# Kernel tuning notes

Hardware: AMD Instinct MI355X
Metric: run time of the kernel (lower is better)

The kernel has to match this reference:

```python
import jax, jax.numpy as jnp
import numpy as np

D_MODEL = 1024
N_HEADS = 16
HEAD_DIM = D_MODEL // N_HEADS


def setup_inputs() -> dict:
    key = jax.random.key(0)
    k_x, k_qkv, k_out = jax.random.split(key, 3)
    B, T = 4, 2048
    x = jax.random.normal(k_x, (B, T, D_MODEL), dtype=jnp.float32)
    # nn.Linear weight is (out, in); we store transposed (in, out) for x @ W
    s = 1.0 / np.sqrt(D_MODEL)
    W_qkv = jax.random.uniform(k_qkv, (D_MODEL, 3 * D_MODEL), dtype=jnp.float32, minval=-s, maxval=s)
    W_out = jax.random.uniform(k_out, (D_MODEL, D_MODEL), dtype=jnp.float32, minval=-s, maxval=s)
    return {"x": x, "W_qkv": W_qkv, "W_out": W_out}


def reference(x, W_qkv, W_out):
    B, T, C = x.shape
    H, Dh = N_HEADS, HEAD_DIM
    qkv = x @ W_qkv                                   # (B,T,3C)
    q, k, v = jnp.split(qkv, 3, axis=-1)
    # (B,T,C) -> (B,H,T,Dh)
    def split_heads(t):
        return t.reshape(B, T, H, Dh).transpose(0, 2, 1, 3)
    q, k, v = split_heads(q), split_heads(k), split_heads(v)
    scale = 1.0 / np.sqrt(Dh).astype(np.float32)
    scores = jnp.einsum('bhqd,bhkd->bhqk', q, k) * scale  # (B,H,T,T)
    causal = jnp.triu(jnp.ones((T, T), dtype=bool), k=1)   # True above diag
    scores = jnp.where(causal, -jnp.inf, scores)
    attn = jax.nn.softmax(scores, axis=-1)
    out = jnp.einsum('bhqk,bhkd->bhqd', attn, v)       # (B,H,T,Dh)
    out = out.transpose(0, 2, 1, 3).reshape(B, T, C)
    return out @ W_out
```

## Files before the change

### kernel.cpp

```cpp
#include <hip/hip_runtime.h>
#include <stdint.h>

#define T_ 2048
#define BB_ 4

typedef __bf16 bf16x8 __attribute__((ext_vector_type(8)));
typedef float f32x4 __attribute__((ext_vector_type(4)));
typedef unsigned short u16x8 __attribute__((ext_vector_type(8)));
typedef unsigned int u32x2 __attribute__((ext_vector_type(2)));
typedef unsigned int u32x4 __attribute__((ext_vector_type(4)));

__device__ __forceinline__ unsigned short f2b(float f) {
    unsigned int u = __builtin_bit_cast(unsigned int, f);
    return (unsigned short)((u + 0x7fffu + ((u >> 16) & 1u)) >> 16);
}

__device__ __forceinline__ unsigned cvt_pk(float lo, float hi) {
    unsigned r;
    asm("v_cvt_pk_bf16_f32 %0, %1, %2" : "=v"(r) : "v"(lo), "v"(hi));
    return r;
}

__device__ __forceinline__ void gload16(const void* g, const void* lds) {
    __builtin_amdgcn_global_load_lds(
        (__attribute__((address_space(1))) void*)(uintptr_t)g,
        (__attribute__((address_space(3))) void*)(uintptr_t)(unsigned int)(uintptr_t)lds,
        16, 0, 0);
}

__device__ __forceinline__ bf16x8 ld_b8(const unsigned short* p) {
    return *(const bf16x8*)p;
}

#define MFMA16(a, b, c) __builtin_amdgcn_mfma_f32_16x16x32_bf16((a), (b), (c), 0, 0, 0)
#define SB() __builtin_amdgcn_sched_barrier(0)

__device__ __forceinline__ void cvtT_body(const float* __restrict__ W,
                                          unsigned short* __restrict__ WT, int K,
                                          int N, int bid, int tid,
                                          unsigned short (*t_)[72]) {
    const int nt = bid % (N / 64), kt = bid / (N / 64);
    const int r = tid >> 2, c = (tid & 3) * 16;
    const float* src = W + (size_t)(kt * 64 + r) * N + nt * 64 + c;
#pragma unroll
    for (int j = 0; j < 16; j += 4) {
        float4 v = *(const float4*)(src + j);
        t_[r][c + j + 0] = f2b(v.x);
        t_[r][c + j + 1] = f2b(v.y);
        t_[r][c + j + 2] = f2b(v.z);
        t_[r][c + j + 3] = f2b(v.w);
    }
    __syncthreads();
    unsigned short* dst = WT + (size_t)(nt * 64 + r) * K + kt * 64 + c;
#pragma unroll
    for (int j = 0; j < 16; ++j) dst[j] = t_[c + j][r];
}

__global__ __launch_bounds__(256) void k_prep(
    const float* __restrict__ x, const float* __restrict__ Wqkv,
    const float* __restrict__ Wout, unsigned short* __restrict__ xb,
    unsigned short* __restrict__ wqkvT, unsigned short* __restrict__ woutT) {
    __shared__ unsigned short t_[64][72];
    const int bid = blockIdx.x, tid = threadIdx.x;
    if (bid < 768) {
        cvtT_body(Wqkv, wqkvT, 1024, 3072, bid, tid, t_);
    } else if (bid < 1024) {
        cvtT_body(Wout, woutT, 1024, 1024, bid - 768, tid, t_);
    } else {
        int i = ((bid - 1024) * 256 + tid) * 4;
        const int stride = 2048 * 256 * 4;
        for (; i < BB_ * T_ * 1024; i += stride) {
            const float4 v = *(const float4*)(x + i);
            *(ushort4*)(xb + i) = make_ushort4(f2b(v.x), f2b(v.y), f2b(v.z), f2b(v.w));
        }
    }
}

__global__ __launch_bounds__(512, 4) void k_gemm32(
    const unsigned short* __restrict__ A, const unsigned short* __restrict__ Bt,
    unsigned short* __restrict__ qkv, unsigned short* __restrict__ vt2) {
    constexpr int K = 1024, NT = K / 32;
    __shared__ unsigned short Abuf[3][8192];
    __shared__ unsigned short Bbuf[3][4096];
    const int tid = threadIdx.x;
    const int lane = tid & 63, wid = tid >> 6;
    const int wr = wid >> 1, wc = wid & 1;
    const int l4 = lane >> 4, l15 = lane & 15;
    const int m0 = blockIdx.y * 256, n0 = blockIdx.x * 128;

    int arow[2], acol[2];
#pragma unroll
    for (int c = 0; c < 2; ++c) {
        const int lb = c * 8192 + tid * 16;
        const int r2 = lb >> 7;
        const int w = (lb & 127) ^ ((r2 & 7) << 4);
        arow[c] = r2 * 2 + (w >> 6);
        acol[c] = (w & 63) >> 1;
    }
    int brow, bcol;
    {
        const int lb = tid * 16;
        const int r2 = lb >> 7;
        const int w = (lb & 127) ^ ((r2 & 7) << 4);
        brow = r2 * 2 + (w >> 6);
        bcol = (w & 63) >> 1;
    }

    f32x4 acc[4][4] = {};

    auto STAGE = [&](int t, int d) {
        gload16(A + (size_t)(m0 + arow[0]) * K + t * 32 + acol[0], &Abuf[d][tid * 8]);
        gload16(A + (size_t)(m0 + arow[1]) * K + t * 32 + acol[1],
                &Abuf[d][4096 + tid * 8]);
        gload16(Bt + (size_t)(n0 + brow) * K + t * 32 + bcol, &Bbuf[d][tid * 8]);
    };

    auto rd = [&](const unsigned short* base, int R) {
        int byte = (R >> 1) * 128 + (R & 1) * 64 + l4 * 16;
        byte ^= ((R >> 1) & 7) << 4;
        return (const unsigned short*)((const char*)base + byte);
    };

    STAGE(0, 0);
    STAGE(1, 1);
    int d = 0;
    for (int t = 0; t < NT; ++t) {
        if (t == NT - 1)
            asm volatile("s_waitcnt vmcnt(0)" ::: "memory");
        else
            asm volatile("s_waitcnt vmcnt(3)" ::: "memory");
        SB();
        __builtin_amdgcn_s_barrier();
        SB();
        const int dn = (d + 2 >= 3) ? d - 1 : d + 2;
        if (t + 2 < NT) STAGE(t + 2, dn);
        SB();
        bf16x8 af[4], bfr[4];
#pragma unroll
        for (int m = 0; m < 4; ++m)
            af[m] = ld_b8(rd(&Abuf[d][0], wr * 64 + m * 16 + l15));
#pragma unroll
        for (int n = 0; n < 4; ++n)
            bfr[n] = ld_b8(rd(&Bbuf[d][0], wc * 64 + n * 16 + l15));
        __builtin_amdgcn_s_setprio(1);
#pragma unroll
        for (int m = 0; m < 4; ++m)
#pragma unroll
            for (int n = 0; n < 4; ++n)
                acc[m][n] = MFMA16(af[m], bfr[n], acc[m][n]);
        __builtin_amdgcn_s_setprio(0);
        d = (d + 1 == 3) ? 0 : d + 1;
    }

    const int crow0 = m0 + wr * 64 + l4 * 4;
    const int ccol0 = n0 + wc * 64 + l15;
    if (n0 >= 2048) {
#pragma unroll
        for (int m = 0; m < 4; ++m)
#pragma unroll
            for (int n = 0; n < 4; ++n) {
                const int row = crow0 + m * 16;
                const int c = ccol0 + n * 16 - 2048;
                const int b = row >> 11, tt = row & 2047;
                const int h = c >> 6, dh = c & 63;
                ushort4 o;
                o.x = f2b(acc[m][n][0]);
                o.y = f2b(acc[m][n][1]);
                o.z = f2b(acc[m][n][2]);
                o.w = f2b(acc[m][n][3]);
                *(ushort4*)(vt2 + (size_t)(b * 16 + h) * 131072 + (tt >> 2) * 256 +
                            dh * 4) = o;
            }
    } else {
#pragma unroll
        for (int m = 0; m < 4; ++m)
#pragma unroll
            for (int n = 0; n < 4; ++n)
#pragma unroll
                for (int r = 0; r < 4; ++r)
                    qkv[(size_t)(crow0 + m * 16 + r) * 3072 + ccol0 + n * 16] =
                        f2b(acc[m][n][r]);
    }
}

__global__ __launch_bounds__(512, 2) void k_gemm256(
    const unsigned short* __restrict__ A, const unsigned short* __restrict__ Bt,
    float* __restrict__ Cv) {
    constexpr int K = 1024, NT = K / 64, NCOLS = 1024;
    __shared__ unsigned short Abuf[3][2][8192];
    __shared__ unsigned short Bbuf[3][8192];
    const int tid = threadIdx.x;
    const int lane = tid & 63, wid = tid >> 6;
    const int wr = wid >> 1, wc = wid & 1;
    const int l4 = lane >> 4, l15 = lane & 15;
    const int m0 = blockIdx.y * 256, n0 = blockIdx.x * 128;

    const int se0 = tid * 8, se1 = tid * 8 + 4096;
    const int r0_ = se0 >> 6, c0_ = (se0 & 63) ^ ((r0_ & 7) << 3);
    const int r1_ = se1 >> 6, c1_ = (se1 & 63) ^ ((r1_ & 7) << 3);

    f32x4 acc[4][4] = {};

    auto STAGE1 = [&](int t, int d) {
        const unsigned short* as = A + (size_t)m0 * K + t * 64;
        gload16(as + (size_t)r0_ * K + c0_, &Abuf[d][0][se0]);
        gload16(as + (size_t)r1_ * K + c1_, &Abuf[d][0][se1]);
        const unsigned short* bs = Bt + (size_t)n0 * K + t * 64;
        gload16(bs + (size_t)r0_ * K + c0_, &Bbuf[d][se0]);
    };
    auto STAGE2 = [&](int t, int d) {
        const unsigned short* as = A + (size_t)(m0 + 128) * K + t * 64;
        gload16(as + (size_t)r0_ * K + c0_, &Abuf[d][1][se0]);
        gload16(as + (size_t)r1_ * K + c1_, &Abuf[d][1][se1]);
        const unsigned short* bs = Bt + (size_t)n0 * K + t * 64;
        gload16(bs + (size_t)r1_ * K + c1_, &Bbuf[d][se1]);
    };

    auto swz = [](const unsigned short* base, int row, int col) {
        int byte = row * 128 + col * 2;
        byte ^= (row & 7) << 4;
        return (const unsigned short*)((const char*)base + byte);
    };

    STAGE1(0, 0);
    STAGE2(0, 0);
    STAGE1(1, 1);
    STAGE2(1, 1);
    int d = 0;
    for (int t = 0; t < NT; ++t) {
        if (t == NT - 1)
            asm volatile("s_waitcnt vmcnt(0)" ::: "memory");
        else
            asm volatile("s_waitcnt vmcnt(6)" ::: "memory");
        SB();
        __builtin_amdgcn_s_barrier();
        SB();
        const int dn = (d + 2 >= 3) ? d - 1 : d + 2;
        if (t + 2 < NT) STAGE1(t + 2, dn);
        SB();
        const unsigned short* Ah = &Abuf[d][wr >> 1][0];
        const unsigned short* Bh = &Bbuf[d][0];
        bf16x8 af[2][4], bfr[2][4];
#pragma unroll
        for (int ks = 0; ks < 2; ++ks) {
#pragma unroll
            for (int m = 0; m < 4; ++m)
                af[ks][m] =
                    ld_b8(swz(Ah, (wr & 1) * 64 + m * 16 + l15, ks * 32 + l4 * 8));
#pragma unroll
            for (int n = 0; n < 4; ++n)
                bfr[ks][n] = ld_b8(swz(Bh, wc * 64 + n * 16 + l15, ks * 32 + l4 * 8));
        }
        __builtin_amdgcn_s_setprio(1);
#pragma unroll
        for (int m = 0; m < 4; ++m)
#pragma unroll
            for (int n = 0; n < 4; ++n)
                acc[m][n] = MFMA16(af[0][m], bfr[0][n], acc[m][n]);
        __builtin_amdgcn_s_setprio(0);
        SB();
        if (t + 2 < NT) STAGE2(t + 2, dn);
        SB();
        __builtin_amdgcn_s_setprio(1);
#pragma unroll
        for (int m = 0; m < 4; ++m)
#pragma unroll
            for (int n = 0; n < 4; ++n)
                acc[m][n] = MFMA16(af[1][m], bfr[1][n], acc[m][n]);
        __builtin_amdgcn_s_setprio(0);
        d = (d + 1 == 3) ? 0 : d + 1;
    }

    const int crow0 = m0 + wr * 64 + l4 * 4;
    const int ccol0 = n0 + wc * 64 + l15;
#pragma unroll
    for (int m = 0; m < 4; ++m)
#pragma unroll
        for (int n = 0; n < 4; ++n)
#pragma unroll
            for (int r = 0; r < 4; ++r)
                Cv[(size_t)(crow0 + m * 16 + r) * NCOLS + ccol0 + n * 16] =
                    acc[m][n][r];
}

__global__ __launch_bounds__(512) void k_attn(const unsigned short* __restrict__ qkv,
                                              const unsigned short* __restrict__ vt2,
                                              unsigned short* __restrict__ ao) {
    __shared__ unsigned short Ks[2 * 4096];
    __shared__ unsigned short Vs[2 * 4096];
    const int bh = blockIdx.x & 63;
    const int p = blockIdx.x >> 6;
    const int b = bh >> 4, h = bh & 15;
    const int tid = threadIdx.x, lane = tid & 63, w = tid >> 6;
    const int l4 = lane >> 4, l15 = lane & 15;
    const int wrow = w * 16 + l15;

    const int sr0 = w * 8 + (lane >> 3);
    const int scol = 8 * ((lane & 7) ^ (lane >> 3));
    const unsigned short* Kg = qkv + (size_t)(b * T_) * 3072 + 1024 + h * 64;

    const unsigned short* Vg = vt2 + (size_t)bh * 131072;
    const int sv = w * 2 + (lane >> 5);
    const unsigned short* vsrcw =
        Vg + (4 * (sv & 3) + (sv >> 2)) * 256 + (lane & 31) * 8;

    const u32x4 onesw = {0x3f803f80u, 0x3f803f80u, 0x3f803f80u, 0x3f803f80u};
    const bf16x8 ones = __builtin_bit_cast(bf16x8, onesw);

    for (int half = 0; half < 2; ++half) {
        const int qq = half ? p : 15 - p;

        const unsigned short* qb =
            qkv + (size_t)(b * T_ + qq * 128 + wrow) * 3072 + h * 64;
        bf16x8 qf0, qf1;
        {
            const bf16x8 r0 = ld_b8(qb + l4 * 8);
            const bf16x8 r1 = ld_b8(qb + 32 + l4 * 8);
#pragma unroll
            for (int j = 0; j < 8; ++j) {
                qf0[j] = (__bf16)((float)r0[j] * 0.18033688f);
                qf1[j] = (__bf16)((float)r1[j] * 0.18033688f);
            }
        }

        f32x4 o[4] = {};
        f32x4 o_l = {};

        auto STAGE = [&](int kt, int bi) {
            gload16(Kg + (size_t)(kt * 64 + sr0) * 3072 + scol,
                    Ks + bi * 4096 + w * 512);
            gload16(vsrcw + (size_t)kt * 4096, Vs + bi * 4096 + w * 512);
        };

        auto COMPUTE = [&](int bi, int dk) {
            const unsigned short* Kb = Ks + bi * 4096;
            const unsigned short* Vb = Vs + bi * 4096;
            float tv[4][4];
            __builtin_amdgcn_s_setprio(1);
#pragma unroll
            for (int i = 0; i < 4; ++i) {
                const int key = i * 16 + l15;
                const int sw = (key & 7) << 4;
                const bf16x8 kf0 = ld_b8(Kb + (key * 128 + ((l4 * 16) ^ sw)) / 2);
                const bf16x8 kf1 = ld_b8(Kb + (key * 128 + ((l4 * 16 + 64) ^ sw)) / 2);
                f32x4 sacc = {};
                sacc = MFMA16(kf0, qf0, sacc);
                sacc = MFMA16(kf1, qf1, sacc);
#pragma unroll
                for (int r = 0; r < 4; ++r) tv[i][r] = sacc[r];
            }
            __builtin_amdgcn_s_setprio(0);
            if (dk >= 0) {
                const int base = dk * 64 - wrow;
#pragma unroll
                for (int i = 0; i < 4; ++i)
#pragma unroll
                    for (int r = 0; r < 4; ++r)
                        if (base + i * 16 + l4 * 4 + r > 0) tv[i][r] = -1e30f;
            }
            unsigned pw[8];
#pragma unroll
            for (int i = 0; i < 4; ++i) {
                float pv[4];
#pragma unroll
                for (int r = 0; r < 4; ++r) pv[r] = __builtin_amdgcn_exp2f(tv[i][r]);
                pw[i * 2 + 0] = cvt_pk(pv[0], pv[1]);
                pw[i * 2 + 1] = cvt_pk(pv[2], pv[3]);
            }
            __builtin_amdgcn_s_setprio(1);
#pragma unroll
            for (int st = 0; st < 2; ++st) {
                const u32x4 pk = {pw[st * 4 + 0], pw[st * 4 + 1], pw[st * 4 + 2],
                                  pw[st * 4 + 3]};
                const bf16x8 pf = __builtin_bit_cast(bf16x8, pk);
                o_l = MFMA16(pf, ones, o_l);
#pragma unroll
                for (int ni = 0; ni < 4; ++ni) {
                    const unsigned short* vb =
                        Vb + (l4 * 4 + st * 2) * 256 + (ni * 16 + l15) * 4;
                    const u32x2 va = *(const u32x2*)vb;
                    const u32x2 vc = *(const u32x2*)(vb + 256);
                    const u32x4 vv = {va.x, va.y, vc.x, vc.y};
                    const bf16x8 vf = __builtin_bit_cast(bf16x8, vv);
                    o[ni] = MFMA16(pf, vf, o[ni]);
                }
            }
            __builtin_amdgcn_s_setprio(0);
        };

        const int NTI = 2 * qq + 1;
        __syncthreads();
        STAGE(0, 0);
        __syncthreads();
        for (int kt = 0; kt < NTI; ++kt) {
            STAGE(kt + 1, (kt + 1) & 1);
            COMPUTE(kt & 1, kt - 2 * qq);
            __syncthreads();
        }
        COMPUTE(NTI & 1, 1);

        unsigned short* aop =
            ao + (size_t)(b * T_ + qq * 128 + w * 16) * 1024 + h * 64;
#pragma unroll
        for (int r = 0; r < 4; ++r) {
            const float inv = 1.0f / o_l[r];
#pragma unroll
            for (int ni = 0; ni < 4; ++ni)
                aop[(size_t)(l4 * 4 + r) * 1024 + ni * 16 + l15] = f2b(o[ni][r] * inv);
        }
    }
}

extern "C" void kernel_launch(void* const* d_in, const int* in_sizes, int n_in,
                              void* d_out, int out_size, void* d_ws, size_t ws_size,
                              hipStream_t stream) {
    (void)in_sizes; (void)n_in; (void)out_size; (void)ws_size;
    const float* x = (const float*)d_in[0];
    const float* Wqkv = (const float*)d_in[1];
    const float* Wout = (const float*)d_in[2];
    char* ws = (char*)d_ws;
    unsigned short* xb = (unsigned short*)(ws + 0);
    unsigned short* wqkvT = (unsigned short*)(ws + 16777216);
    unsigned short* woutT = (unsigned short*)(ws + 23068672);
    unsigned short* qkvb = (unsigned short*)(ws + 25165824);
    unsigned short* vt2 = (unsigned short*)(ws + 75497472);
    unsigned short* ao = (unsigned short*)(ws + 92274688);

    k_prep<<<3072, 256, 0, stream>>>(x, Wqkv, Wout, xb, wqkvT, woutT);
    k_gemm32<<<dim3(24, 32), 512, 0, stream>>>(xb, wqkvT, qkvb, vt2);
    k_attn<<<512, 512, 0, stream>>>(qkvb, vt2, ao);
    k_gemm256<<<dim3(8, 32), 512, 0, stream>>>(ao, woutT, (float*)d_out);
}
```

Measured before the change: 143.9 us.

## Retile QKV GEMM to 128x192 blocks with a 2x4 wave layout

Changes the QKV projection GEMM tile from 256x128 to 128x192, giving 1024 blocks instead of 768, with 8 waves arranged 2x4, each computing 64x48. The staging loads become uneven: only the first four waves issue the extra B load, and the waitcnt depth is set per wave to match. The epilogue now decides per 16-column fragment whether to write the V-transposed layout, because a 192-wide tile can straddle the Q/K and V boundary. The goal is better wave-quantisation across CUs, at the cost of lower arithmetic intensity per tile and divergent load counts between waves.

```diff
diff --git a/kernel.cpp b/kernel.cpp
--- a/kernel.cpp
+++ b/kernel.cpp
@@ -76,43 +76,43 @@
     }
 }
 
-__global__ __launch_bounds__(512, 4) void k_gemm32(
+__global__ __launch_bounds__(512, 4) void k_gemm192(
     const unsigned short* __restrict__ A, const unsigned short* __restrict__ Bt,
     unsigned short* __restrict__ qkv, unsigned short* __restrict__ vt2) {
     constexpr int K = 1024, NT = K / 32;
-    __shared__ unsigned short Abuf[3][8192];
-    __shared__ unsigned short Bbuf[3][4096];
+    __shared__ unsigned short Abuf[3][4096];
+    __shared__ unsigned short Bbuf[3][6144];
     const int tid = threadIdx.x;
     const int lane = tid & 63, wid = tid >> 6;
-    const int wr = wid >> 1, wc = wid & 1;
+    const int wm = wid >> 2, wn = wid & 3;
     const int l4 = lane >> 4, l15 = lane & 15;
-    const int m0 = blockIdx.y * 256, n0 = blockIdx.x * 128;
-
-    int arow[2], acol[2];
-#pragma unroll
-    for (int c = 0; c < 2; ++c) {
-        const int lb = c * 8192 + tid * 16;
-        const int r2 = lb >> 7;
-        const int w = (lb & 127) ^ ((r2 & 7) << 4);
-        arow[c] = r2 * 2 + (w >> 6);
-        acol[c] = (w & 63) >> 1;
-    }
-    int brow, bcol;
+    const int m0 = blockIdx.y * 128, n0 = blockIdx.x * 192;
+
+    int ar, ac;
     {
         const int lb = tid * 16;
         const int r2 = lb >> 7;
         const int w = (lb & 127) ^ ((r2 & 7) << 4);
-        brow = r2 * 2 + (w >> 6);
-        bcol = (w & 63) >> 1;
-    }
-
-    f32x4 acc[4][4] = {};
+        ar = r2 * 2 + (w >> 6);
+        ac = (w & 63) >> 1;
+    }
+    int br1, bc1;
+    {
+        const int lb = 8192 + tid * 16;
+        const int r2 = lb >> 7;
+        const int w = (lb & 127) ^ ((r2 & 7) << 4);
+        br1 = r2 * 2 + (w >> 6);
+        bc1 = (w & 63) >> 1;
+    }
+
+    f32x4 acc[4][3] = {};
 
     auto STAGE = [&](int t, int d) {
-        gload16(A + (size_t)(m0 + arow[0]) * K + t * 32 + acol[0], &Abuf[d][tid * 8]);
-        gload16(A + (size_t)(m0 + arow[1]) * K + t * 32 + acol[1],
-                &Abuf[d][4096 + tid * 8]);
-        gload16(Bt + (size_t)(n0 + brow) * K + t * 32 + bcol, &Bbuf[d][tid * 8]);
+        gload16(A + (size_t)(m0 + ar) * K + t * 32 + ac, &Abuf[d][tid * 8]);
+        gload16(Bt + (size_t)(n0 + ar) * K + t * 32 + ac, &Bbuf[d][tid * 8]);
+        if (wid < 4)
+            gload16(Bt + (size_t)(n0 + br1) * K + t * 32 + bc1,
+                    &Bbuf[d][4096 + tid * 8]);
     };
 
     auto rd = [&](const unsigned short* base, int R) {
@@ -125,44 +125,48 @@
     STAGE(1, 1);
     int d = 0;
     for (int t = 0; t < NT; ++t) {
-        if (t == NT - 1)
+        if (t == NT - 1) {
             asm volatile("s_waitcnt vmcnt(0)" ::: "memory");
-        else
+        } else if (wid < 4) {
             asm volatile("s_waitcnt vmcnt(3)" ::: "memory");
+        } else {
+            asm volatile("s_waitcnt vmcnt(2)" ::: "memory");
+        }
         SB();
         __builtin_amdgcn_s_barrier();
         SB();
         const int dn = (d + 2 >= 3) ? d - 1 : d + 2;
         if (t + 2 < NT) STAGE(t + 2, dn);
         SB();
-        bf16x8 af[4], bfr[4];
+        bf16x8 af[4], bfr[3];
 #pragma unroll
         for (int m = 0; m < 4; ++m)
-            af[m] = ld_b8(rd(&Abuf[d][0], wr * 64 + m * 16 + l15));
-#pragma unroll
-        for (int n = 0; n < 4; ++n)
-            bfr[n] = ld_b8(rd(&Bbuf[d][0], wc * 64 + n * 16 + l15));
+            af[m] = ld_b8(rd(&Abuf[d][0], wm * 64 + m * 16 + l15));
+#pragma unroll
+        for (int n = 0; n < 3; ++n)
+            bfr[n] = ld_b8(rd(&Bbuf[d][0], wn * 48 + n * 16 + l15));
         __builtin_amdgcn_s_setprio(1);
 #pragma unroll
         for (int m = 0; m < 4; ++m)
 #pragma unroll
-            for (int n = 0; n < 4; ++n)
+            for (int n = 0; n < 3; ++n)
                 acc[m][n] = MFMA16(af[m], bfr[n], acc[m][n]);
         __builtin_amdgcn_s_setprio(0);
         d = (d + 1 == 3) ? 0 : d + 1;
     }
 
-    const int crow0 = m0 + wr * 64 + l4 * 4;
-    const int ccol0 = n0 + wc * 64 + l15;
-    if (n0 >= 2048) {
-#pragma unroll
-        for (int m = 0; m < 4; ++m)
-#pragma unroll
-            for (int n = 0; n < 4; ++n) {
-                const int row = crow0 + m * 16;
-                const int c = ccol0 + n * 16 - 2048;
+    const int crow0 = m0 + wm * 64 + l4 * 4;
+    const int ccol0 = n0 + wn * 48 + l15;
+#pragma unroll
+    for (int m = 0; m < 4; ++m)
+#pragma unroll
+        for (int n = 0; n < 3; ++n) {
+            const int row = crow0 + m * 16;
+            const int c = ccol0 + n * 16;
+            if (c - l15 >= 2048) {
+                const int cv = c - 2048;
                 const int b = row >> 11, tt = row & 2047;
-                const int h = c >> 6, dh = c & 63;
+                const int h = cv >> 6, dh = cv & 63;
                 ushort4 o;
                 o.x = f2b(acc[m][n][0]);
                 o.y = f2b(acc[m][n][1]);
@@ -170,17 +174,12 @@
                 o.w = f2b(acc[m][n][3]);
                 *(ushort4*)(vt2 + (size_t)(b * 16 + h) * 131072 + (tt >> 2) * 256 +
                             dh * 4) = o;
-            }
-    } else {
-#pragma unroll
-        for (int m = 0; m < 4; ++m)
-#pragma unroll
-            for (int n = 0; n < 4; ++n)
+            } else {
 #pragma unroll
                 for (int r = 0; r < 4; ++r)
-                    qkv[(size_t)(crow0 + m * 16 + r) * 3072 + ccol0 + n * 16] =
-                        f2b(acc[m][n][r]);
-    }
+                    qkv[(size_t)(row + r) * 3072 + c] = f2b(acc[m][n][r]);
+            }
+        }
 }
 
 __global__ __launch_bounds__(512, 2) void k_gemm256(
@@ -427,7 +426,7 @@
     unsigned short* ao = (unsigned short*)(ws + 92274688);
 
     k_prep<<<3072, 256, 0, stream>>>(x, Wqkv, Wout, xb, wqkvT, woutT);
-    k_gemm32<<<dim3(24, 32), 512, 0, stream>>>(xb, wqkvT, qkvb, vt2);
+    k_gemm192<<<dim3(16, 64), 512, 0, stream>>>(xb, wqkvT, qkvb, vt2);
     k_attn<<<512, 512, 0, stream>>>(qkvb, vt2, ao);
     k_gemm256<<<dim3(8, 32), 512, 0, stream>>>(ao, woutT, (float*)d_out);
 }
```

Measured after the change: 148.7 us. +3.3%, slower.
